# Optimization experiments

Hardware: AMD Instinct MI355X
Metric: run time of the kernel (lower is better)

The kernel has to match this reference:

```python
import jax, jax.numpy as jnp
import numpy as np

N_TOK = 16384   # total tokens (batch*seq)
H = 2048        # hidden_size
I = 768         # moe_intermediate_size (per-expert MLP width)
TOPK = 8        # num_experts_per_tok


def setup_inputs() -> dict:
    key = jax.random.key(0)
    ks = jax.random.split(key, 7)
    hidden_states = jax.random.normal(ks[0], (N_TOK, H), dtype=jnp.float32)
    # expert_mask[j, k] != 0 means token k selected this expert at top-k slot j
    expert_mask = jax.random.randint(ks[1], (TOPK, N_TOK), 0, 2, dtype=jnp.int32)
    routing_weights = jax.random.uniform(ks[2], (N_TOK, TOPK), dtype=jnp.float32)
    final_hidden_states = jax.random.normal(ks[3], (N_TOK, H), dtype=jnp.float32)
    gate_w = jax.random.normal(ks[4], (I, H), dtype=jnp.float32) * 0.02
    up_w = jax.random.normal(ks[5], (I, H), dtype=jnp.float32) * 0.02
    down_w = jax.random.normal(ks[6], (H, I), dtype=jnp.float32) * 0.02
    return {
        "hidden_states": hidden_states,
        "expert_mask": expert_mask,
        "routing_weights": routing_weights,
        "final_hidden_states": final_hidden_states,
        "gate_w": gate_w,
        "up_w": up_w,
        "down_w": down_w,
    }


def reference(hidden_states, expert_mask, routing_weights, final_hidden_states,
              gate_w, up_w, down_w):
    # forward_expert: gather selected tokens, SwiGLU MLP, scale by routing weight,
    # scatter-add into final_hidden_states. Equivalent jit-friendly form: the
    # combined routing weight per token is w[k] = sum_j mask[j,k]*routing_weights[k,j]
    # (tokens selected multiple times are summed, matching index_add_ semantics),
    # and unselected tokens get w[k]=0 so they contribute nothing.
    g = hidden_states @ gate_w.T                       # [N, I]
    u = hidden_states @ up_w.T                         # [N, I]
    y = (jax.nn.silu(g) * u) @ down_w.T                # [N, H]
    w = jnp.einsum('jk,kj->k', expert_mask.astype(y.dtype), routing_weights)  # [N]
    return final_hidden_states + y * w[:, None]
```

## Files before the change

### kernel.cpp

```cpp
#include <hip/hip_runtime.h>
#include <stdint.h>

#define NTOK 16384
#define HD   2048
#define ID   768
#define TOPK 8

typedef __bf16 bf16x8 __attribute__((ext_vector_type(8)));
typedef float  floatx4 __attribute__((ext_vector_type(4)));
typedef unsigned short ushort8 __attribute__((ext_vector_type(8)));

__device__ __forceinline__ unsigned short f32_to_bf16_rne(float f) {
    union { float f; uint32_t u; } v; v.f = f;
    uint32_t u = v.u;
    u += 0x7FFFu + ((u >> 16) & 1u);
    return (unsigned short)(u >> 16);
}

#define GLD_LDS(gsrc, ldst)                                                              \
    __builtin_amdgcn_global_load_lds(                                                    \
        (const __attribute__((address_space(1))) uint32_t*)(const void*)(gsrc),          \
        (__attribute__((address_space(3))) uint32_t*)(void*)(ldst), 16, 0, 0)

template<int VM> __device__ __forceinline__ void wait_vm() {
    if constexpr (VM == 8)      asm volatile("s_waitcnt vmcnt(8)" ::: "memory");
    else if constexpr (VM == 4) asm volatile("s_waitcnt vmcnt(4)" ::: "memory");
    else                        asm volatile("s_waitcnt vmcnt(0)" ::: "memory");
}
#define BARRIER() do { asm volatile("" ::: "memory");              \
                       __builtin_amdgcn_s_barrier();               \
                       asm volatile("" ::: "memory"); } while (0)

__global__ __launch_bounds__(256) void compute_w_kernel(const int* __restrict__ mask,
                                                        const float* __restrict__ rw,
                                                        float* __restrict__ w) {
    int k = blockIdx.x * 256 + threadIdx.x;
    if (k >= NTOK) return;
    float acc = 0.f;
#pragma unroll
    for (int j = 0; j < TOPK; ++j)
        acc += (float)mask[j * NTOK + k] * rw[k * TOPK + j];
    w[k] = acc;
}

__global__ __launch_bounds__(256) void convert_hs_kernel(const float* __restrict__ src,
                                                         unsigned short* __restrict__ dst) {
    size_t i = (size_t)blockIdx.x * 256 + threadIdx.x;
    const float4* s = (const float4*)src;
    float4 a = s[2 * i], b = s[2 * i + 1];
    ushort8 o;
    o[0] = f32_to_bf16_rne(a.x); o[1] = f32_to_bf16_rne(a.y);
    o[2] = f32_to_bf16_rne(a.z); o[3] = f32_to_bf16_rne(a.w);
    o[4] = f32_to_bf16_rne(b.x); o[5] = f32_to_bf16_rne(b.y);
    o[6] = f32_to_bf16_rne(b.z); o[7] = f32_to_bf16_rne(b.w);
    *(ushort8*)(dst + 8 * i) = o;
}

__global__ __launch_bounds__(256) void convert_w3_kernel(const float* __restrict__ g,
                                                         const float* __restrict__ u,
                                                         const float* __restrict__ d,
                                                         unsigned short* __restrict__ dst) {
    int i = blockIdx.x * 256 + threadIdx.x;
    size_t e = (size_t)i * 8;
    const float* src;
    if (e < (size_t)2 * ID * HD) {
        int rd = (int)(e / HD);
        int c  = (int)(e - (size_t)rd * HD);
        int b = rd >> 4, h = (rd >> 3) & 1, sub = rd & 7;
        src = (h ? u : g) + (size_t)(b * 8 + sub) * HD + c;
    } else {
        src = d + (e - (size_t)2 * ID * HD);
    }
    const float4* s = (const float4*)src;
    float4 a = s[0], bq = s[1];
    ushort8 o;
    o[0] = f32_to_bf16_rne(a.x);  o[1] = f32_to_bf16_rne(a.y);
    o[2] = f32_to_bf16_rne(a.z);  o[3] = f32_to_bf16_rne(a.w);
    o[4] = f32_to_bf16_rne(bq.x); o[5] = f32_to_bf16_rne(bq.y);
    o[6] = f32_to_bf16_rne(bq.z); o[7] = f32_to_bf16_rne(bq.w);
    *(ushort8*)(dst + e) = o;
}

__global__ __launch_bounds__(512, 1) void gemm_gu_kernel(
    const unsigned short* __restrict__ A,
    const unsigned short* __restrict__ B,
    unsigned short* __restrict__ act) {
    constexpr int K = HD;
    constexpr int NT = K / 64;
    __shared__ __align__(16) unsigned char lds[2][65536];

    const int bid = blockIdx.x, nwg = gridDim.x;
    const int nb = (bid & 7) * (nwg >> 3) + (bid >> 3);
    const int by = nb / 6, bx = nb - by * 6;
    const int row0 = by * 256, col0 = bx * 256;

    const int tid = threadIdx.x, wid = tid >> 6, lane = tid & 63;
    const int wr = wid >> 2, wc = wid & 3;
    const int lrow = lane & 15, q = lane >> 4;
    const int rsw = ((q ^ ((lrow >> 1) & 3)) << 4);

    const int kswz = (((lane & 3) ^ ((lane >> 3) & 3)) << 3);
    const int srow = wid * 16 + (lane >> 2);
    const unsigned short* sA[2];
    const unsigned short* sB[2];
#pragma unroll
    for (int rr = 0; rr < 2; ++rr) {
        sA[rr] = A + (size_t)(row0 + rr * 128 + srow) * K + kswz;
        sB[rr] = B + (size_t)(col0 + rr * 128 + srow) * K + kswz;
    }

#define STAGE_A(sb, ks, kt) do {                                                            \
        GLD_LDS(sA[0] + (kt) * 64 + (ks) * 32, lds[sb] + (ks) * 16384 + wid * 1024);        \
        GLD_LDS(sA[1] + (kt) * 64 + (ks) * 32, lds[sb] + (ks) * 16384 + 8192 + wid * 1024); \
    } while (0)
#define STAGE_B(sb, ks, kt) do {                                                            \
        GLD_LDS(sB[0] + (kt) * 64 + (ks) * 32, lds[sb] + 32768 + (ks) * 16384 + wid * 1024);\
        GLD_LDS(sB[1] + (kt) * 64 + (ks) * 32, lds[sb] + 32768 + (ks) * 16384 + 8192 + wid * 1024); \
    } while (0)

#define READ_A(sb, ks) do { const unsigned char* rgn = lds[sb] + (ks) * 16384;              \
        _Pragma("unroll")                                                                   \
        for (int m = 0; m < 8; ++m)                                                         \
            af[m] = *(const bf16x8*)(rgn + (wr * 128 + m * 16 + lrow) * 64 + rsw);          \
    } while (0)
#define READ_B(sb, ks) do { const unsigned char* rgn = lds[sb] + 32768 + (ks) * 16384;      \
        _Pragma("unroll")                                                                   \
        for (int n = 0; n < 4; ++n)                                                         \
            bb[n] = *(const bf16x8*)(rgn + (wc * 64 + n * 16 + lrow) * 64 + rsw);           \
    } while (0)
#define MFMA_NH(nh) do {                                                                    \
        __builtin_amdgcn_s_setprio(1);                                                      \
        _Pragma("unroll")                                                                   \
        for (int m = 0; m < 8; ++m)                                                         \
            _Pragma("unroll")                                                               \
            for (int j = 0; j < 2; ++j)                                                     \
                acc[m][(nh) * 2 + j] = __builtin_amdgcn_mfma_f32_16x16x32_bf16(af[m], bb[(nh) * 2 + j], acc[m][(nh) * 2 + j], 0, 0, 0); \
        __builtin_amdgcn_s_setprio(0);                                                      \
    } while (0)

    floatx4 acc[8][4];
#pragma unroll
    for (int m = 0; m < 8; ++m)
#pragma unroll
        for (int n = 0; n < 4; ++n) acc[m][n] = (floatx4){0.f, 0.f, 0.f, 0.f};
    bf16x8 af[8], bb[4];

    STAGE_A(0, 0, 0);
    STAGE_B(0, 0, 0);
    STAGE_A(0, 1, 0);
    STAGE_B(0, 1, 0);
    wait_vm<4>();
    BARRIER();

    for (int t = 0; t < NT - 1; ++t) {
        const int s = t & 1, sn = s ^ 1;
        READ_A(s, 0); READ_B(s, 0);
        STAGE_A(sn, 0, t + 1);
        MFMA_NH(0);
        BARRIER();
        STAGE_B(sn, 0, t + 1);
        MFMA_NH(1);
        wait_vm<4>();
        BARRIER();
        READ_A(s, 1); READ_B(s, 1);
        STAGE_A(sn, 1, t + 1);
        MFMA_NH(0);
        BARRIER();
        STAGE_B(sn, 1, t + 1);
        MFMA_NH(1);
        wait_vm<4>();
        BARRIER();
    }
    {
        const int s = (NT - 1) & 1;
        READ_A(s, 0); READ_B(s, 0);
        MFMA_NH(0);
        BARRIER();
        MFMA_NH(1);
        wait_vm<0>();
        BARRIER();
        READ_A(s, 1); READ_B(s, 1);
        MFMA_NH(0);
        MFMA_NH(1);
    }
#undef STAGE_A
#undef STAGE_B
#undef READ_A
#undef READ_B
#undef MFMA_NH

#pragma unroll
    for (int m = 0; m < 8; ++m) {
        const int rowb = row0 + wr * 128 + m * 16 + q * 4;
        float sv[4][4];
#pragma unroll
        for (int n = 0; n < 4; ++n)
#pragma unroll
            for (int r = 0; r < 4; ++r) {
                const float gf = acc[m][n][r];
                const float uf = __shfl_xor(gf, 8, 64);
                const float sig = __builtin_amdgcn_rcpf(1.f + __expf(-gf));
                sv[n][r] = gf * sig * uf;
            }
        if ((lrow & 8) == 0) {
            const int ib0 = (col0 >> 1) + wc * 32 + lrow;
#pragma unroll
            for (int n = 0; n < 4; ++n)
#pragma unroll
                for (int r = 0; r < 4; ++r)
                    act[(size_t)(rowb + r) * ID + ib0 + n * 8] = f32_to_bf16_rne(sv[n][r]);
        }
    }
}

__global__ __launch_bounds__(256, 2) void gemm_down_kernel(
    const unsigned short* __restrict__ A,
    const unsigned short* __restrict__ B,
    const float* __restrict__ fin,
    const float* __restrict__ wtok,
    float* __restrict__ out) {
    constexpr int K = ID;
    constexpr int NT = K / 64;
    __shared__ __align__(16) unsigned char lds[2][32768];

    const int bid = blockIdx.x, nwg = gridDim.x;
    const int nb = (bid & 7) * (nwg >> 3) + (bid >> 3);
    const int bx = nb & 15, by = nb >> 4;
    const int row0 = by * 128, col0 = bx * 128;

    const int tid = threadIdx.x, wid = tid >> 6, lane = tid & 63;
    const int wr = wid >> 1, wc = wid & 1;
    const int lrow = lane & 15, q = lane >> 4;

    const int srow = wid * 8 + (lane >> 3);
    const int sk = (((lane & 7) ^ ((lane >> 3) & 7)) << 3);
    const unsigned short* sA[4];
    const unsigned short* sB[4];
#pragma unroll
    for (int r = 0; r < 4; ++r) {
        sA[r] = A + (size_t)(row0 + r * 32 + srow) * K + sk;
        sB[r] = B + (size_t)(col0 + r * 32 + srow) * K + sk;
    }

#define STAGE_T(sb, kt) do {                                                    \
        _Pragma("unroll")                                                       \
        for (int r = 0; r < 4; ++r)                                             \
            GLD_LDS(sA[r] + (kt) * 64, lds[sb] + r * 4096 + wid * 1024);        \
        _Pragma("unroll")                                                       \
        for (int r = 0; r < 4; ++r)                                             \
            GLD_LDS(sB[r] + (kt) * 64, lds[sb] + 16384 + r * 4096 + wid * 1024);\
    } while (0)

    floatx4 acc[4][4];
#pragma unroll
    for (int m = 0; m < 4; ++m)
#pragma unroll
        for (int n = 0; n < 4; ++n) acc[m][n] = (floatx4){0.f, 0.f, 0.f, 0.f};
    bf16x8 af[4], bb[4];

    STAGE_T(0, 0);

    for (int t = 0; t < NT; ++t) {
        const int s = t & 1;
        if (t + 1 < NT) {
            STAGE_T(s ^ 1, t + 1);
            wait_vm<8>();
        } else {
            wait_vm<0>();
        }
        BARRIER();
        const unsigned char* la = lds[s];
        const unsigned char* lb = lds[s] + 16384;
#pragma unroll
        for (int ks = 0; ks < 2; ++ks) {
#pragma unroll
            for (int m = 0; m < 4; ++m)
                af[m] = *(const bf16x8*)(la + (wr * 64 + m * 16 + lrow) * 128 +
                                         (((ks * 4 + q) ^ (lrow & 7)) << 4));
#pragma unroll
            for (int n = 0; n < 4; ++n)
                bb[n] = *(const bf16x8*)(lb + (wc * 64 + n * 16 + lrow) * 128 +
                                         (((ks * 4 + q) ^ (lrow & 7)) << 4));
            __builtin_amdgcn_s_setprio(1);
#pragma unroll
            for (int m = 0; m < 4; ++m)
#pragma unroll
                for (int n = 0; n < 4; ++n)
                    acc[m][n] = __builtin_amdgcn_mfma_f32_16x16x32_bf16(af[m], bb[n], acc[m][n], 0, 0, 0);
            __builtin_amdgcn_s_setprio(0);
        }
        BARRIER();
    }
#undef STAGE_T

#pragma unroll
    for (int m = 0; m < 4; ++m)
#pragma unroll
        for (int r = 0; r < 4; ++r) {
            const int row = row0 + wr * 64 + m * 16 + q * 4 + r;
            const float wv = wtok[row];
#pragma unroll
            for (int n = 0; n < 4; ++n) {
                const int col = col0 + wc * 64 + n * 16 + lrow;
                out[(size_t)row * HD + col] = fin[(size_t)row * HD + col] + wv * acc[m][n][r];
            }
        }
}

extern "C" void kernel_launch(void* const* d_in, const int* in_sizes, int n_in,
                              void* d_out, int out_size, void* d_ws, size_t ws_size,
                              hipStream_t stream) {
    const float* hs   = (const float*)d_in[0];
    const int*   mask = (const int*)d_in[1];
    const float* rw   = (const float*)d_in[2];
    const float* fin  = (const float*)d_in[3];
    const float* gw   = (const float*)d_in[4];
    const float* uw   = (const float*)d_in[5];
    const float* dw   = (const float*)d_in[6];
    float* out = (float*)d_out;

    char* ws = (char*)d_ws;
    unsigned short* hs_b   = (unsigned short*)ws; ws += (size_t)NTOK * HD * 2;
    unsigned short* wcat_b = (unsigned short*)ws; ws += (size_t)3 * ID * HD * 2;
    unsigned short* act_b  = (unsigned short*)ws; ws += (size_t)NTOK * ID * 2;
    float* wtok = (float*)ws;
    unsigned short* down_b = wcat_b + (size_t)2 * ID * HD;

    compute_w_kernel<<<NTOK / 256, 256, 0, stream>>>(mask, rw, wtok);
    convert_hs_kernel<<<(NTOK * HD / 8) / 256, 256, 0, stream>>>(hs, hs_b);
    convert_w3_kernel<<<(3 * ID * HD / 8) / 256, 256, 0, stream>>>(gw, uw, dw, wcat_b);

    gemm_gu_kernel<<<384, 512, 0, stream>>>(hs_b, wcat_b, act_b);

    gemm_down_kernel<<<2048, 256, 0, stream>>>(act_b, down_b, fin, wtok, out);
}
```

Before: 236.0 us.

## Shrink gate/up GEMM tile to 256x128 with K=32 steps for multi-block occupancy

Reworks the gate/up GEMM from a 256x256 tile with a 64-wide K step and split half-step pipelining into a 256x128 tile with a 32-wide K step and a simpler double-buffered loop. LDS per block drops from 128KB to 48KB and launch bounds allow several blocks per CU, doubling the grid to 768 blocks. The aim is better latency hiding through occupancy instead of intra-block software pipelining. In exchange, each block reuses less data per load, and the per-iteration barriers and thinner MFMA work per step may expose more synchronisation overhead.

```diff
diff --git a/kernel.cpp b/kernel.cpp
--- a/kernel.cpp
+++ b/kernel.cpp
@@ -24,7 +24,7 @@
 
 template<int VM> __device__ __forceinline__ void wait_vm() {
     if constexpr (VM == 8)      asm volatile("s_waitcnt vmcnt(8)" ::: "memory");
-    else if constexpr (VM == 4) asm volatile("s_waitcnt vmcnt(4)" ::: "memory");
+    else if constexpr (VM == 3) asm volatile("s_waitcnt vmcnt(3)" ::: "memory");
     else                        asm volatile("s_waitcnt vmcnt(0)" ::: "memory");
 }
 #define BARRIER() do { asm volatile("" ::: "memory");              \
@@ -81,117 +81,76 @@
     *(ushort8*)(dst + e) = o;
 }
 
-__global__ __launch_bounds__(512, 1) void gemm_gu_kernel(
+__global__ __launch_bounds__(512, 4) void gemm_gu_kernel(
     const unsigned short* __restrict__ A,
     const unsigned short* __restrict__ B,
     unsigned short* __restrict__ act) {
     constexpr int K = HD;
-    constexpr int NT = K / 64;
-    __shared__ __align__(16) unsigned char lds[2][65536];
+    constexpr int NT = K / 32;
+    __shared__ __align__(16) unsigned char lds[2][24576];
 
     const int bid = blockIdx.x, nwg = gridDim.x;
     const int nb = (bid & 7) * (nwg >> 3) + (bid >> 3);
-    const int by = nb / 6, bx = nb - by * 6;
-    const int row0 = by * 256, col0 = bx * 256;
+    const int by = nb / 12, bx = nb - by * 12;
+    const int row0 = by * 256, col0 = bx * 128;
 
     const int tid = threadIdx.x, wid = tid >> 6, lane = tid & 63;
-    const int wr = wid >> 2, wc = wid & 3;
+    const int wr = wid >> 1, wc = wid & 1;
     const int lrow = lane & 15, q = lane >> 4;
     const int rsw = ((q ^ ((lrow >> 1) & 3)) << 4);
 
     const int kswz = (((lane & 3) ^ ((lane >> 3) & 3)) << 3);
     const int srow = wid * 16 + (lane >> 2);
-    const unsigned short* sA[2];
-    const unsigned short* sB[2];
-#pragma unroll
-    for (int rr = 0; rr < 2; ++rr) {
-        sA[rr] = A + (size_t)(row0 + rr * 128 + srow) * K + kswz;
-        sB[rr] = B + (size_t)(col0 + rr * 128 + srow) * K + kswz;
-    }
-
-#define STAGE_A(sb, ks, kt) do {                                                            \
-        GLD_LDS(sA[0] + (kt) * 64 + (ks) * 32, lds[sb] + (ks) * 16384 + wid * 1024);        \
-        GLD_LDS(sA[1] + (kt) * 64 + (ks) * 32, lds[sb] + (ks) * 16384 + 8192 + wid * 1024); \
+    const unsigned short* s0 = A + (size_t)(row0 + srow) * K + kswz;
+    const unsigned short* s1 = A + (size_t)(row0 + 128 + srow) * K + kswz;
+    const unsigned short* s2 = B + (size_t)(col0 + srow) * K + kswz;
+
+#define STAGE(sb, kt) do {                                                  \
+        GLD_LDS(s0 + (kt) * 32, lds[sb] + wid * 1024);                      \
+        GLD_LDS(s1 + (kt) * 32, lds[sb] + 8192 + wid * 1024);               \
+        GLD_LDS(s2 + (kt) * 32, lds[sb] + 16384 + wid * 1024);              \
     } while (0)
-#define STAGE_B(sb, ks, kt) do {                                                            \
-        GLD_LDS(sB[0] + (kt) * 64 + (ks) * 32, lds[sb] + 32768 + (ks) * 16384 + wid * 1024);\
-        GLD_LDS(sB[1] + (kt) * 64 + (ks) * 32, lds[sb] + 32768 + (ks) * 16384 + 8192 + wid * 1024); \
-    } while (0)
-
-#define READ_A(sb, ks) do { const unsigned char* rgn = lds[sb] + (ks) * 16384;              \
-        _Pragma("unroll")                                                                   \
-        for (int m = 0; m < 8; ++m)                                                         \
-            af[m] = *(const bf16x8*)(rgn + (wr * 128 + m * 16 + lrow) * 64 + rsw);          \
-    } while (0)
-#define READ_B(sb, ks) do { const unsigned char* rgn = lds[sb] + 32768 + (ks) * 16384;      \
-        _Pragma("unroll")                                                                   \
-        for (int n = 0; n < 4; ++n)                                                         \
-            bb[n] = *(const bf16x8*)(rgn + (wc * 64 + n * 16 + lrow) * 64 + rsw);           \
-    } while (0)
-#define MFMA_NH(nh) do {                                                                    \
-        __builtin_amdgcn_s_setprio(1);                                                      \
-        _Pragma("unroll")                                                                   \
-        for (int m = 0; m < 8; ++m)                                                         \
-            _Pragma("unroll")                                                               \
-            for (int j = 0; j < 2; ++j)                                                     \
-                acc[m][(nh) * 2 + j] = __builtin_amdgcn_mfma_f32_16x16x32_bf16(af[m], bb[(nh) * 2 + j], acc[m][(nh) * 2 + j], 0, 0, 0); \
-        __builtin_amdgcn_s_setprio(0);                                                      \
-    } while (0)
-
-    floatx4 acc[8][4];
-#pragma unroll
-    for (int m = 0; m < 8; ++m)
+
+    floatx4 acc[4][4];
+#pragma unroll
+    for (int m = 0; m < 4; ++m)
 #pragma unroll
         for (int n = 0; n < 4; ++n) acc[m][n] = (floatx4){0.f, 0.f, 0.f, 0.f};
-    bf16x8 af[8], bb[4];
-
-    STAGE_A(0, 0, 0);
-    STAGE_B(0, 0, 0);
-    STAGE_A(0, 1, 0);
-    STAGE_B(0, 1, 0);
-    wait_vm<4>();
-    BARRIER();
-
-    for (int t = 0; t < NT - 1; ++t) {
-        const int s = t & 1, sn = s ^ 1;
-        READ_A(s, 0); READ_B(s, 0);
-        STAGE_A(sn, 0, t + 1);
-        MFMA_NH(0);
-        BARRIER();
-        STAGE_B(sn, 0, t + 1);
-        MFMA_NH(1);
-        wait_vm<4>();
-        BARRIER();
-        READ_A(s, 1); READ_B(s, 1);
-        STAGE_A(sn, 1, t + 1);
-        MFMA_NH(0);
-        BARRIER();
-        STAGE_B(sn, 1, t + 1);
-        MFMA_NH(1);
-        wait_vm<4>();
-        BARRIER();
-    }
-    {
-        const int s = (NT - 1) & 1;
-        READ_A(s, 0); READ_B(s, 0);
-        MFMA_NH(0);
-        BARRIER();
-        MFMA_NH(1);
-        wait_vm<0>();
-        BARRIER();
-        READ_A(s, 1); READ_B(s, 1);
-        MFMA_NH(0);
-        MFMA_NH(1);
-    }
-#undef STAGE_A
-#undef STAGE_B
-#undef READ_A
-#undef READ_B
-#undef MFMA_NH
-
-#pragma unroll
-    for (int m = 0; m < 8; ++m) {
-        const int rowb = row0 + wr * 128 + m * 16 + q * 4;
+    bf16x8 af[4], bb[4];
+
+    STAGE(0, 0);
+
+    for (int t = 0; t < NT; ++t) {
+        const int s = t & 1;
+        if (t + 1 < NT) {
+            STAGE(s ^ 1, t + 1);
+            wait_vm<3>();
+        } else {
+            wait_vm<0>();
+        }
+        BARRIER();
+        const unsigned char* la = lds[s];
+        const unsigned char* lb = lds[s] + 16384;
+#pragma unroll
+        for (int m = 0; m < 4; ++m)
+            af[m] = *(const bf16x8*)(la + (wr * 64 + m * 16 + lrow) * 64 + rsw);
+#pragma unroll
+        for (int n = 0; n < 4; ++n)
+            bb[n] = *(const bf16x8*)(lb + (wc * 64 + n * 16 + lrow) * 64 + rsw);
+        __builtin_amdgcn_s_setprio(1);
+#pragma unroll
+        for (int m = 0; m < 4; ++m)
+#pragma unroll
+            for (int n = 0; n < 4; ++n)
+                acc[m][n] = __builtin_amdgcn_mfma_f32_16x16x32_bf16(af[m], bb[n], acc[m][n], 0, 0, 0);
+        __builtin_amdgcn_s_setprio(0);
+        BARRIER();
+    }
+#undef STAGE
+
+#pragma unroll
+    for (int m = 0; m < 4; ++m) {
+        const int rowb = row0 + wr * 64 + m * 16 + q * 4;
         float sv[4][4];
 #pragma unroll
         for (int n = 0; n < 4; ++n)
@@ -203,7 +162,7 @@
                 sv[n][r] = gf * sig * uf;
             }
         if ((lrow & 8) == 0) {
-            const int ib0 = (col0 >> 1) + wc * 32 + lrow;
+            const int ib0 = (col0 >> 1) + wc * 32 + (lrow & 7);
 #pragma unroll
             for (int n = 0; n < 4; ++n)
 #pragma unroll
@@ -330,7 +289,7 @@
     convert_hs_kernel<<<(NTOK * HD / 8) / 256, 256, 0, stream>>>(hs, hs_b);
     convert_w3_kernel<<<(3 * ID * HD / 8) / 256, 256, 0, stream>>>(gw, uw, dw, wcat_b);
 
-    gemm_gu_kernel<<<384, 512, 0, stream>>>(hs_b, wcat_b, act_b);
+    gemm_gu_kernel<<<768, 512, 0, stream>>>(hs_b, wcat_b, act_b);
 
     gemm_down_kernel<<<2048, 256, 0, stream>>>(act_b, down_b, fin, wtok, out);
 }
```

Result: no change. 234.5 us (-0.7%).
